# Kernel optimization log

Measured on AMD Instinct MI355X. Metric: run time of the kernel, lower is better.

The kernel has to match this reference:

```python
import jax, jax.numpy as jnp
import numpy as np

BETA = 0.25
EPS = 1e-12  # torch F.normalize eps


def l2norm(v):
    n = jnp.linalg.norm(v, axis=-1, keepdims=True)
    return v / jnp.maximum(n, EPS)


def setup_inputs() -> dict:
    key = jax.random.key(0)
    k1, k2 = jax.random.split(key)
    x = jax.random.normal(k1, (32, 1024, 256), dtype=jnp.float32)
    embedding = jax.random.normal(k2, (8192, 256), dtype=jnp.float32)
    return {"x": x, "embedding": embedding}


def reference(x, embedding):
    D = embedding.shape[1]
    # normalize flattened inputs and codebook (use_norm=True)
    zf = l2norm(x.reshape(-1, D))            # [B*T, D]
    cb = l2norm(embedding)                   # [N, D]
    # pairwise squared L2: |a|^2 - 2 a.b + |b|^2  (same math as broadcasted diff)
    d = (jnp.sum(zf * zf, axis=-1, keepdims=True)
         - 2.0 * (zf @ cb.T)
         + jnp.sum(cb * cb, axis=-1)[None, :])  # [B*T, N]
    idx = jnp.argmin(d, axis=1).reshape(x.shape[:-1])  # [B, T]
    z_q = embedding[idx]                     # lookup from UN-normalized table
    z_qn = l2norm(z_q)
    z_n = l2norm(x)
    loss = (BETA * jnp.mean((jax.lax.stop_gradient(z_qn) - z_n) ** 2)
            + jnp.mean((z_qn - jax.lax.stop_gradient(z_n)) ** 2))
    # straight-through estimator
    z_out = x + jax.lax.stop_gradient(z_qn - x)
    return z_out, loss, idx
```

## Files before the change

kernel.cpp:

```cpp
#include <hip/hip_runtime.h>


#define M_ROWS 32768
#define N_CODES 8192
#define DIM 256
#define NT 64
#define BUF_B 16384

typedef short v8s __attribute__((ext_vector_type(8)));
typedef _Float16 v8h __attribute__((ext_vector_type(8)));
typedef float v4f __attribute__((ext_vector_type(4)));
typedef unsigned int uint;
typedef unsigned long long ull;

__device__ __forceinline__ unsigned short f2h(float f) {
    union { _Float16 h; unsigned short u; } c;
    c.h = (_Float16)f;
    return c.u;
}
__device__ __forceinline__ uint umax2(uint a, uint b) { return a > b ? a : b; }
__device__ __forceinline__ uint umax3(uint a, uint b, uint c) {
    uint d; asm("v_max3_u32 %0, %1, %2, %3" : "=v"(d) : "v"(a), "v"(b), "v"(c)); return d;
}
__device__ __forceinline__ uint umed3(uint a, uint b, uint c) {
    uint d; asm("v_med3_u32 %0, %1, %2, %3" : "=v"(d) : "v"(a), "v"(b), "v"(c)); return d;
}
__device__ __forceinline__ int swz(int u, int r) {
    return (u & 24) | ((u ^ r) & 7);
}
__device__ __forceinline__ void dma16(const void* g, void* l) {
    __builtin_amdgcn_global_load_lds(
        (const __attribute__((address_space(1))) unsigned int*)g,
        (__attribute__((address_space(3))) unsigned int*)l, 16, 0, 0);
}

__global__ __launch_bounds__(256) void normalize_kernel(
        const float* __restrict__ emb, const float* __restrict__ x,
        float* __restrict__ cb, unsigned short* __restrict__ cbh,
        unsigned short* __restrict__ zfh, uint* __restrict__ count) {
    if (blockIdx.x == 0 && threadIdx.x == 0) *count = 0u;
    int wave = threadIdx.x >> 6, lane = threadIdx.x & 63;
    int rg = blockIdx.x * 4 + wave;
    bool is_cb = rg < N_CODES;
    int r = is_cb ? rg : rg - N_CODES;
    const float* src = is_cb ? emb : x;
    float4 v = *(const float4*)(src + (size_t)r * DIM + lane * 4);
    float ss = v.x * v.x + v.y * v.y + v.z * v.z + v.w * v.w;
    #pragma unroll
    for (int o = 32; o; o >>= 1) ss += __shfl_xor(ss, o);
    float rinv = 1.0f / fmaxf(sqrtf(ss), 1e-12f);
    float4 o4; o4.x = v.x * rinv; o4.y = v.y * rinv; o4.z = v.z * rinv; o4.w = v.w * rinv;
    ushort4 b; b.x = f2h(o4.x); b.y = f2h(o4.y); b.z = f2h(o4.z); b.w = f2h(o4.w);
    if (is_cb) {
        *(float4*)(cb + (size_t)r * DIM + lane * 4) = o4;
        int rr = r & 31;
        size_t off = (size_t)r * 512
                   + (size_t)swz(lane >> 1, rr) * 16
                   + (size_t)(lane & 1) * 8;
        *(ushort4*)((char*)cbh + off) = b;
    } else {
        *(ushort4*)(zfh + (size_t)r * DIM + lane * 4) = b;
    }
}

__global__ __launch_bounds__(256, 2) void scan_kernel(
        const unsigned short* __restrict__ zfh,
        const unsigned short* __restrict__ cbh,
        uint* __restrict__ cand) {
    __shared__ __align__(16) char lds[4 * BUF_B];
    int tid = threadIdx.x, w = tid >> 6, lane = tid & 63;
    int m = lane & 15, g = lane >> 4;
    int rb = blockIdx.x >> 2, quarter = blockIdx.x & 3;
    int r0 = rb * 256 + w * 64;
    const v4f C2 = {2.f, 2.f, 2.f, 2.f};

    v8h a[4][8];
    #pragma unroll
    for (int h = 0; h < 4; ++h) {
        const unsigned short* ap = zfh + (size_t)(r0 + h * 16 + m) * DIM + g * 8;
        #pragma unroll
        for (int c = 0; c < 8; ++c) a[h][c] = *(const v8h*)(ap + c * 32);
    }
    asm volatile("" ::: "memory");

    const char* cb_base = (const char*)cbh + ((size_t)quarter << 20);
    int wq = 4 * w;

    int roff[8];
    #pragma unroll
    for (int c = 0; c < 8; ++c)
        roff[c] = m * 512 + swz(4 * c + g, m) * 16;

    #pragma unroll
    for (int tt = 0; tt < 3; ++tt) {
        const char* gsrc = cb_base + (size_t)tt * BUF_B + wq * 1024 + lane * 16;
        char* lb = lds + (tt & 3) * BUF_B + wq * 1024;
        #pragma unroll
        for (int i = 0; i < 4; ++i) dma16(gsrc + i * 1024, lb + i * 1024);
    }

    uint top1[16], top2[16];
    #pragma unroll
    for (int i = 0; i < 16; ++i) { top1[i] = 0u; top2[i] = 0u; }

    for (int t = 0; t < NT; ++t) {
        if (t < NT - 2) asm volatile("s_waitcnt vmcnt(8)" ::: "memory");
        else            asm volatile("s_waitcnt vmcnt(0)" ::: "memory");
        __builtin_amdgcn_s_barrier();
        if (t + 3 < NT) {
            const char* gsrc = cb_base + (size_t)(t + 3) * BUF_B + wq * 1024 + lane * 16;
            char* lb = lds + ((t + 3) & 3) * BUF_B + wq * 1024;
            #pragma unroll
            for (int i = 0; i < 4; ++i) dma16(gsrc + i * 1024, lb + i * 1024);
        }
        const char* cbuf = lds + (t & 3) * BUF_B;
        v4f acc[2][4];
        __builtin_amdgcn_s_setprio(1);
        #pragma unroll
        for (int s2 = 0; s2 < 2; ++s2) {
            #pragma unroll
            for (int c = 0; c < 8; ++c) {
                v8h b = *(const v8h*)(cbuf + s2 * 8192 + roff[c]);
                #pragma unroll
                for (int h = 0; h < 4; ++h) {
                    v4f cin = (c == 0) ? C2 : acc[s2][h];
                    acc[s2][h] = __builtin_amdgcn_mfma_f32_16x16x32_f16(a[h][c], b, cin, 0, 0, 0);
                }
            }
        }
        __builtin_amdgcn_s_setprio(0);
        uint gt0 = (uint)(quarter * 128 + 2 * t);
        uint gt1 = gt0 + 1u;
        #pragma unroll
        for (int i = 0; i < 16; ++i) {
            float s0 = acc[0][i >> 2][i & 3];
            float s1 = acc[1][i >> 2][i & 3];
            uint k0 = (__float_as_uint(s0) & 0xFFFFFE00u) | gt0;
            uint k1 = (__float_as_uint(s1) & 0xFFFFFE00u) | gt1;
            uint old1 = top1[i];
            top1[i] = umax3(old1, k0, k1);
            top2[i] = umax2(top2[i], umed3(old1, k0, k1));
        }
    }

    #pragma unroll
    for (int i = 0; i < 16; ++i) {
        int h = i >> 2, q = i & 3;
        int row = r0 + h * 16 + g * 4 + q;
        uint2 v; v.x = top1[i]; v.y = top2[i];
        *(uint2*)(cand + (size_t)row * 128 + (quarter * 16 + m) * 2) = v;
    }
}

__global__ __launch_bounds__(256, 4) void rescore_kernel(
        const float* __restrict__ x, const float* __restrict__ cb,
        const uint* __restrict__ cand, float* __restrict__ out,
        float* __restrict__ out_idx, double* __restrict__ lossp) {
    __shared__ int s_surv[4][128];
    int w = threadIdx.x >> 6, lane = threadIdx.x & 63;
    int r = blockIdx.x * 4 + w;
    float4 xv = *(const float4*)(x + (size_t)r * DIM + lane * 4);
    uint2 kk = *(const uint2*)(cand + (size_t)r * 128 + lane * 2);

    float ss = xv.x * xv.x + xv.y * xv.y + xv.z * xv.z + xv.w * xv.w;
    #pragma unroll
    for (int o = 32; o; o >>= 1) ss += __shfl_xor(ss, o);
    float rinv = 1.0f / fmaxf(sqrtf(ss), 1e-12f);
    float4 z4; z4.x = xv.x * rinv; z4.y = xv.y * rinv; z4.z = xv.z * rinv; z4.w = xv.w * rinv;

    float kf0 = __uint_as_float(kk.x & 0xFFFFFE00u);
    float kf1 = __uint_as_float(kk.y & 0xFFFFFE00u);
    int code0 = (int)(kk.x & 0x1FFu) * 16 + (lane & 15);
    int code1 = (int)(kk.y & 0x1FFu) * 16 + (lane & 15);
    float mykey = fmaxf(kf0, kf1);
    int mycode = (kf0 >= kf1) ? code0 : code1;
    float kmax = mykey;
    #pragma unroll
    for (int o = 32; o; o >>= 1) kmax = fmaxf(kmax, __shfl_xor(kmax, o));
    ull mm = __ballot(mykey == kmax);
    int spec = __shfl(mycode, (int)__builtin_ctzll(mm));
    float4 cspec = *(const float4*)(cb + (size_t)spec * DIM + lane * 4);

    float thr = kmax - 0.008f;
    bool p0 = kf0 >= thr, p1 = kf1 >= thr;
    ull m0 = __ballot(p0), m1 = __ballot(p1);
    ull lt = (1ull << lane) - 1ull;
    int ns0 = __popcll(m0);
    int ns = ns0 + __popcll(m1);
    if (p0) s_surv[w][__popcll(m0 & lt)] = code0;
    if (p1) s_surv[w][ns0 + __popcll(m1 & lt)] = code1;

    int bestj;
    if (ns == 1) {
        bestj = spec;
    } else {
        float d1 = 3.0e38f; int jj = 0x7fffffff;
        int nsl = ns < 64 ? ns : 64;
        for (int s = 0; s < nsl; ++s) {
            int j = s_surv[w][s];
            float4 c4 = *(const float4*)(cb + (size_t)j * DIM + lane * 4);
            float d = c4.x * (c4.x - 2.f * z4.x) + c4.y * (c4.y - 2.f * z4.y)
                    + c4.z * (c4.z - 2.f * z4.z) + c4.w * (c4.w - 2.f * z4.w);
            #pragma unroll
            for (int o = 32; o; o >>= 1) d += __shfl_xor(d, o);
            if (lane == s) { d1 = d; jj = j; }
        }
        if (ns > 64) {
            float d2 = 3.0e38f; int jj2 = 0x7fffffff;
            for (int s = 64; s < ns; ++s) {
                int j = s_surv[w][s];
                float4 c4 = *(const float4*)(cb + (size_t)j * DIM + lane * 4);
                float d = c4.x * (c4.x - 2.f * z4.x) + c4.y * (c4.y - 2.f * z4.y)
                        + c4.z * (c4.z - 2.f * z4.z) + c4.w * (c4.w - 2.f * z4.w);
                #pragma unroll
                for (int o = 32; o; o >>= 1) d += __shfl_xor(d, o);
                if (lane == s - 64) { d2 = d; jj2 = j; }
            }
            if (d2 < d1 || (d2 == d1 && jj2 < jj)) { d1 = d2; jj = jj2; }
        }
        float dmin = d1;
        #pragma unroll
        for (int o = 32; o; o >>= 1) dmin = fminf(dmin, __shfl_xor(dmin, o));
        ull nearm = __ballot(d1 <= dmin + 2e-4f);
        if (__popcll(nearm) == 1) {
            bestj = __shfl(jj, (int)__builtin_ctzll(nearm));
        } else {
            double bestd = 1e300; bestj = 0x7fffffff;
            while (nearm) {
                int b = (int)__builtin_ctzll(nearm); nearm &= nearm - 1;
                int jc = __shfl(jj, b);
                float4 c4 = *(const float4*)(cb + (size_t)jc * DIM + lane * 4);
                double p = (double)c4.x * ((double)c4.x - 2.0 * (double)z4.x)
                         + (double)c4.y * ((double)c4.y - 2.0 * (double)z4.y)
                         + (double)c4.z * ((double)c4.z - 2.0 * (double)z4.z)
                         + (double)c4.w * ((double)c4.w - 2.0 * (double)z4.w);
                #pragma unroll
                for (int o = 32; o; o >>= 1) p += __shfl_xor(p, o);
                if (p < bestd || (p == bestd && jc < bestj)) { bestd = p; bestj = jc; }
            }
        }
    }
    float4 c4;
    if (bestj == spec) c4 = cspec;
    else c4 = *(const float4*)(cb + (size_t)bestj * DIM + lane * 4);
    *(float4*)(out + (size_t)r * DIM + lane * 4) = c4;
    double dx = (double)c4.x - (double)z4.x, dy = (double)c4.y - (double)z4.y;
    double dz = (double)c4.z - (double)z4.z, dw = (double)c4.w - (double)z4.w;
    double lp = dx * dx + dy * dy + dz * dz + dw * dw;
    #pragma unroll
    for (int o = 32; o; o >>= 1) lp += __shfl_xor(lp, o);
    if (lane == 0) { lossp[r] = lp; out_idx[r] = (float)bestj; }
}

__global__ __launch_bounds__(256) void loss_kernel(
        const double* __restrict__ lossp, float* __restrict__ out,
        double* __restrict__ partial, uint* __restrict__ count) {
    __shared__ double sm[256];
    __shared__ int is_last;
    int b = blockIdx.x, tid = threadIdx.x;
    double2 v = *(const double2*)(lossp + (size_t)b * 512 + tid * 2);
    sm[tid] = v.x + v.y;
    __syncthreads();
    for (int o = 128; o; o >>= 1) {
        if (tid < o) sm[tid] += sm[tid + o];
        __syncthreads();
    }
    if (tid == 0) {
        partial[b] = sm[0];
        __threadfence();
        uint old = atomicAdd(count, 1u);
        is_last = (old == 63u);
    }
    __syncthreads();
    if (is_last && tid < 64) {
        __threadfence();
        double p = partial[tid];
        #pragma unroll
        for (int o = 32; o; o >>= 1) p += __shfl_xor(p, o);
        if (tid == 0)
            out[0] = (float)(p * (1.25 / (double)(M_ROWS * DIM)));
    }
}

extern "C" void kernel_launch(void* const* d_in, const int* in_sizes, int n_in,
                              void* d_out, int out_size, void* d_ws, size_t ws_size,
                              hipStream_t stream) {
    const float* x   = (const float*)d_in[0];
    const float* emb = (const float*)d_in[1];
    float* out = (float*)d_out;
    char* ws = (char*)d_ws;

    float*          cb    = (float*)(ws);
    unsigned short* cbh   = (unsigned short*)(ws + (8u  << 20));
    unsigned short* zfh   = (unsigned short*)(ws + (12u << 20));
    uint*           cand  = (uint*)(ws + (28u << 20));
    double*         lossp = (double*)(ws + (44u << 20));
    double*         partial = (double*)(ws + (44u << 20) + (512u << 10));
    uint*           count = (uint*)(ws + (44u << 20) + (513u << 10));

    normalize_kernel<<<(N_CODES + M_ROWS) / 4, 256, 0, stream>>>(emb, x, cb, cbh, zfh, count);
    scan_kernel<<<512, 256, 0, stream>>>(zfh, cbh, cand);
    rescore_kernel<<<M_ROWS / 4, 256, 0, stream>>>(x, cb, cand,
                                                   out, out + ((size_t)M_ROWS * DIM + 1), lossp);
    loss_kernel<<<64, 256, 0, stream>>>(lossp, out + (size_t)M_ROWS * DIM, partial, count);
}
```

Before: 232.0 us.

## Split codebook tile between LDS staging and direct global register loads

Each 16 KB codebook tile is now split. One half is staged through LDS with async DMA, and the other half is read by every wave straight from global memory into registers. This halves the LDS footprint and the DMA traffic per iteration, aiming to cut LDS pressure and barrier-bound staging. The cost is that each wave redundantly fetches the global half, and that load latency is exposed inside the compute loop. The waits on those in-order loads may also force earlier prefetches to drain, weakening the pipeline.

```diff
diff --git a/kernel.cpp b/kernel.cpp
--- a/kernel.cpp
+++ b/kernel.cpp
@@ -5,7 +5,8 @@
 #define N_CODES 8192
 #define DIM 256
 #define NT 64
-#define BUF_B 16384
+#define TILE_B 16384
+#define STG_B 8192
 
 typedef short v8s __attribute__((ext_vector_type(8)));
 typedef _Float16 v8h __attribute__((ext_vector_type(8)));
@@ -67,7 +68,7 @@
         const unsigned short* __restrict__ zfh,
         const unsigned short* __restrict__ cbh,
         uint* __restrict__ cand) {
-    __shared__ __align__(16) char lds[4 * BUF_B];
+    __shared__ __align__(16) char lds[4 * STG_B];
     int tid = threadIdx.x, w = tid >> 6, lane = tid & 63;
     int m = lane & 15, g = lane >> 4;
     int rb = blockIdx.x >> 2, quarter = blockIdx.x & 3;
@@ -84,7 +85,7 @@
     asm volatile("" ::: "memory");
 
     const char* cb_base = (const char*)cbh + ((size_t)quarter << 20);
-    int wq = 4 * w;
+    int wq = 2 * w;
 
     int roff[8];
     #pragma unroll
@@ -93,10 +94,10 @@
 
     #pragma unroll
     for (int tt = 0; tt < 3; ++tt) {
-        const char* gsrc = cb_base + (size_t)tt * BUF_B + wq * 1024 + lane * 16;
-        char* lb = lds + (tt & 3) * BUF_B + wq * 1024;
-        #pragma unroll
-        for (int i = 0; i < 4; ++i) dma16(gsrc + i * 1024, lb + i * 1024);
+        const char* gsrc = cb_base + (size_t)tt * TILE_B + wq * 1024 + lane * 16;
+        char* lb = lds + tt * STG_B + wq * 1024;
+        #pragma unroll
+        for (int i = 0; i < 2; ++i) dma16(gsrc + i * 1024, lb + i * 1024);
     }
 
     uint top1[16], top2[16];
@@ -104,28 +105,39 @@
     for (int i = 0; i < 16; ++i) { top1[i] = 0u; top2[i] = 0u; }
 
     for (int t = 0; t < NT; ++t) {
-        if (t < NT - 2) asm volatile("s_waitcnt vmcnt(8)" ::: "memory");
+        if (t < NT - 2) asm volatile("s_waitcnt vmcnt(4)" ::: "memory");
         else            asm volatile("s_waitcnt vmcnt(0)" ::: "memory");
         __builtin_amdgcn_s_barrier();
+
+        const char* gB = cb_base + (size_t)t * TILE_B + STG_B;
+        v8h bg[8];
+        #pragma unroll
+        for (int c = 0; c < 8; ++c) bg[c] = *(const v8h*)(gB + roff[c]);
+
         if (t + 3 < NT) {
-            const char* gsrc = cb_base + (size_t)(t + 3) * BUF_B + wq * 1024 + lane * 16;
-            char* lb = lds + ((t + 3) & 3) * BUF_B + wq * 1024;
+            const char* gsrc = cb_base + (size_t)(t + 3) * TILE_B + wq * 1024 + lane * 16;
+            char* lb = lds + ((t + 3) & 3) * STG_B + wq * 1024;
             #pragma unroll
-            for (int i = 0; i < 4; ++i) dma16(gsrc + i * 1024, lb + i * 1024);
-        }
-        const char* cbuf = lds + (t & 3) * BUF_B;
+            for (int i = 0; i < 2; ++i) dma16(gsrc + i * 1024, lb + i * 1024);
+        }
+        const char* cbuf = lds + (t & 3) * STG_B;
         v4f acc[2][4];
         __builtin_amdgcn_s_setprio(1);
         #pragma unroll
-        for (int s2 = 0; s2 < 2; ++s2) {
+        for (int c = 0; c < 8; ++c) {
+            v8h b = *(const v8h*)(cbuf + roff[c]);
             #pragma unroll
-            for (int c = 0; c < 8; ++c) {
-                v8h b = *(const v8h*)(cbuf + s2 * 8192 + roff[c]);
-                #pragma unroll
-                for (int h = 0; h < 4; ++h) {
-                    v4f cin = (c == 0) ? C2 : acc[s2][h];
-                    acc[s2][h] = __builtin_amdgcn_mfma_f32_16x16x32_f16(a[h][c], b, cin, 0, 0, 0);
-                }
+            for (int h = 0; h < 4; ++h) {
+                v4f cin = (c == 0) ? C2 : acc[0][h];
+                acc[0][h] = __builtin_amdgcn_mfma_f32_16x16x32_f16(a[h][c], b, cin, 0, 0, 0);
+            }
+        }
+        #pragma unroll
+        for (int c = 0; c < 8; ++c) {
+            #pragma unroll
+            for (int h = 0; h < 4; ++h) {
+                v4f cin = (c == 0) ? C2 : acc[1][h];
+                acc[1][h] = __builtin_amdgcn_mfma_f32_16x16x32_f16(a[h][c], bg[c], cin, 0, 0, 0);
             }
         }
         __builtin_amdgcn_s_setprio(0);
```

Measured after the change: 237.9 us. 1.03x slower.
